# Kernel tuning notes

Hardware: AMD Instinct MI355X
Metric: run time of the kernel (lower is better)

## Reference

```python
import jax, jax.numpy as jnp
import numpy as np
from jax import lax

SIGMA = 1.5
KSIZE = 11  # int(6*1.5+1)=10 -> even -> 11
PAD = KSIZE // 2


def _gaussian_kernel_3d(ksize: int, sigma: float, dtype=jnp.float32):
    coords = jnp.arange(ksize, dtype=dtype) - (ksize // 2)
    g = jnp.exp(-(coords ** 2) / (2.0 * sigma ** 2))
    g = g / jnp.sum(g)
    # dense rank-1 separable outer product -> [k, k, k]
    k3 = g[:, None, None] * g[None, :, None] * g[None, None, :]
    return k3


def setup_inputs() -> dict:
    key = jax.random.key(0)
    x = jax.random.normal(key, (4, 1, 160, 192, 192), dtype=jnp.float32)
    return {"x": x}


def reference(x):
    # Faithful to torch: full dense 3D conv with the k^3 Gaussian kernel,
    # 'same' padding of kernel_size//2, single in/out channel.
    k3 = _gaussian_kernel_3d(KSIZE, SIGMA, x.dtype)
    w = k3[None, None]  # [O=1, I=1, kD, kH, kW]
    out = lax.conv_general_dilated(
        x, w,
        window_strides=(1, 1, 1),
        padding=[(PAD, PAD)] * 3,
        dimension_numbers=("NCDHW", "OIDHW", "NCDHW"),
    )
    return out
```

## Files before the change

kernel.cpp:

```cpp
#include <hip/hip_runtime.h>
#include <hip/hip_bf16.h>
#include <math.h>

#define KSIZE 11
#define PAD 5

struct GaussW { float w[KSIZE]; };

#define B_    4
#define D_    160
#define H_    192
#define W_    192
#define W4_   48

typedef float floatx4 __attribute__((ext_vector_type(4)));

#define TW4    16
#define TH     48
#define DCH    5
#define NH     (H_ / TH)
#define NWT    (W_ / (TW4*4))
#define NDC    (D_ / DCH)
#define NBLK_A (B_ * NH * NWT * NDC)
#define INROWS (TH + 10)
#define INW4   (TW4 + 4)
#define IN_STR4 21
#define WT_STR4 17
#define NSTAGE (INROWS * INW4)
#define PSTR4  (H_ * W4_)

static __device__ inline unsigned short f2bf(float f) {
    __hip_bfloat16 h = __float2bfloat16(f);
    return __builtin_bit_cast(unsigned short, h);
}
static __device__ inline float4 bf4_to_f4(ushort4 u) {
    return make_float4(__uint_as_float((unsigned)u.x << 16),
                       __uint_as_float((unsigned)u.y << 16),
                       __uint_as_float((unsigned)u.z << 16),
                       __uint_as_float((unsigned)u.w << 16));
}

__global__ __launch_bounds__(256) void blur_wh3(const float4* __restrict__ src,
                                                ushort4* __restrict__ wsb,
                                                GaussW g) {
    __shared__ __align__(16) float  lds_in[INROWS * IN_STR4 * 4];
    __shared__ __align__(16) ushort4 wtb[INROWS * WT_STR4];

    int bid = blockIdx.x;
    int L = (bid & 7) * (NBLK_A / 8) + (bid >> 3);
    int wx = L % NWT; L /= NWT;
    int hy = L % NH;  L /= NH;
    int dc = L % NDC;
    int b  = L / NDC;

    const int h0  = hy * TH;
    const int w0q = wx * TW4;
    const int d0  = dc * DCH;
    const int tid = threadIdx.x;

    const int wr   = tid >> 2;
    const int wq   = (tid & 3) * 4;
    const bool wact = (wr < INROWS);

    const int c4  = tid & 15;
    const int grp = tid >> 4;

    const float4* pin = src + (b * D_ + d0) * PSTR4;
    ushort4* pout = wsb + (b * D_ + d0) * PSTR4 + (h0 + 3 * grp) * W4_ + w0q + c4;

    float4 pf[5];
    auto issue = [&](const float4* plane) {
#pragma unroll
        for (int j = 0; j < 5; ++j) {
            pf[j] = make_float4(0.f, 0.f, 0.f, 0.f);
            int it = tid + j * 256;
            if (it < NSTAGE) {
                int ir = it / INW4, jc = it - ir * INW4;
                int h = h0 - PAD + ir;
                int q = w0q - 2 + jc;
                if (h >= 0 && h < H_ && q >= 0 && q < W4_)
                    pf[j] = plane[h * W4_ + q];
            }
        }
    };
    auto stage_write = [&]() {
#pragma unroll
        for (int j = 0; j < 5; ++j) {
            int it = tid + j * 256;
            if (it < NSTAGE) {
                int ir = it / INW4, jc = it - ir * INW4;
                *(float4*)&lds_in[(ir * IN_STR4 + jc) * 4] = pf[j];
            }
        }
    };

    issue(pin);
    stage_write();
    issue(pin + PSTR4);
    __syncthreads();

    for (int p = 0; p < DCH; ++p) {
        if (wact) {
            float win[32];
            const float* row = &lds_in[(wr * IN_STR4 + wq) * 4];
#pragma unroll
            for (int u = 0; u < 8; ++u) {
                float4 v = *(const float4*)&row[u * 4];
                win[4*u+0] = v.x; win[4*u+1] = v.y;
                win[4*u+2] = v.z; win[4*u+3] = v.w;
            }
            float o[16];
#pragma unroll
            for (int i = 0; i < 16; ++i) {
                float a = 0.f;
#pragma unroll
                for (int t = 0; t < KSIZE; ++t) a += g.w[t] * win[i + 3 + t];
                o[i] = a;
            }
            ushort4* wrow = &wtb[wr * WT_STR4 + wq];
#pragma unroll
            for (int c = 0; c < 4; ++c)
                wrow[c] = make_ushort4(f2bf(o[4*c]), f2bf(o[4*c+1]),
                                       f2bf(o[4*c+2]), f2bf(o[4*c+3]));
        }
        __syncthreads();

        if (p + 1 < DCH) stage_write();
        if (p + 2 < DCH) issue(pin + (p + 2) * PSTR4);

        {
            float4 a0 = make_float4(0.f,0.f,0.f,0.f);
            float4 a1 = a0, a2 = a0;
#pragma unroll
            for (int j = 0; j < 13; ++j) {
                float4 v = bf4_to_f4(wtb[(3*grp + j) * WT_STR4 + c4]);
                if (j <= 10) {
                    float wt_ = g.w[j];
                    a0.x += wt_*v.x; a0.y += wt_*v.y; a0.z += wt_*v.z; a0.w += wt_*v.w;
                }
                if (j >= 1 && j <= 11) {
                    float wt_ = g.w[j-1];
                    a1.x += wt_*v.x; a1.y += wt_*v.y; a1.z += wt_*v.z; a1.w += wt_*v.w;
                }
                if (j >= 2) {
                    float wt_ = g.w[j-2];
                    a2.x += wt_*v.x; a2.y += wt_*v.y; a2.z += wt_*v.z; a2.w += wt_*v.w;
                }
            }
            ushort4* op = pout + p * PSTR4;
            op[0      ] = make_ushort4(f2bf(a0.x), f2bf(a0.y), f2bf(a0.z), f2bf(a0.w));
            op[W4_    ] = make_ushort4(f2bf(a1.x), f2bf(a1.y), f2bf(a1.z), f2bf(a1.w));
            op[2 * W4_] = make_ushort4(f2bf(a2.x), f2bf(a2.y), f2bf(a2.z), f2bf(a2.w));
        }
        __syncthreads();
    }
}

template <int STR4, int LEN, int CH>
__global__ __launch_bounds__(256) void blur_d_slide(const ushort4* __restrict__ src,
                                                    float4* __restrict__ dst,
                                                    GaussW g, int ncol) {
    int tid = blockIdx.x * blockDim.x + threadIdx.x;
    int col = tid % ncol;
    int chunk = tid / ncol;
    int c0 = chunk * CH;
    int inner = col % STR4;
    int outer = col / STR4;
    int base = outer * (LEN * STR4) + inner;

    float4 ring[KSIZE];
#pragma unroll
    for (int j = 0; j < KSIZE - 1; ++j) {
        int cc = c0 - PAD + j;
        float4 v = make_float4(0.f, 0.f, 0.f, 0.f);
        if (cc >= 0 && cc < LEN) v = bf4_to_f4(src[base + cc * STR4]);
        ring[j] = v;
    }
#pragma unroll
    for (int k = 0; k < CH; ++k) {
        int cc = c0 + k + PAD;
        float4 v = make_float4(0.f, 0.f, 0.f, 0.f);
        if (cc < LEN) v = bf4_to_f4(src[base + cc * STR4]);
        ring[(KSIZE - 1 + k) % KSIZE] = v;

        float4 acc = make_float4(0.f, 0.f, 0.f, 0.f);
#pragma unroll
        for (int t = 0; t < KSIZE; ++t) {
            float4 u = ring[(k + t) % KSIZE];
            float wt = g.w[t];
            acc.x += wt * u.x; acc.y += wt * u.y;
            acc.z += wt * u.z; acc.w += wt * u.w;
        }
        floatx4 av; av.x = acc.x; av.y = acc.y; av.z = acc.z; av.w = acc.w;
        __builtin_nontemporal_store(av, (floatx4*)&dst[base + (c0 + k) * STR4]);
    }
}

__global__ void blur_dense_fallback(const float* __restrict__ src,
                                    float* __restrict__ dst,
                                    GaussW g, int B, int D, int H, int W) {
    long n = (long)B * D * H * W;
    long i = (long)blockIdx.x * blockDim.x + threadIdx.x;
    if (i >= n) return;
    int w = (int)(i % W);
    long r = i / W;
    int h = (int)(r % H); r /= H;
    int d = (int)(r % D);
    int b = (int)(r / D);

    float acc = 0.f;
    for (int td = 0; td < KSIZE; ++td) {
        int dd = d + td - PAD;
        if (dd < 0 || dd >= D) continue;
        for (int th = 0; th < KSIZE; ++th) {
            int hh = h + th - PAD;
            if (hh < 0 || hh >= H) continue;
            float wdh = g.w[td] * g.w[th];
            const float* row = src + (((long)b * D + dd) * H + hh) * W;
            for (int tw = 0; tw < KSIZE; ++tw) {
                int ww = w + tw - PAD;
                if (ww < 0 || ww >= W) continue;
                acc += wdh * g.w[tw] * row[ww];
            }
        }
    }
    dst[i] = acc;
}

extern "C" void kernel_launch(void* const* d_in, const int* in_sizes, int n_in,
                              void* d_out, int out_size, void* d_ws, size_t ws_size,
                              hipStream_t stream) {
    const float* x = (const float*)d_in[0];
    float* out = (float*)d_out;
    (void)in_sizes; (void)n_in; (void)out_size;

    const long n = (long)B_ * D_ * H_ * W_;

    GaussW g;
    {
        double tmp[KSIZE], s = 0.0;
        for (int i = 0; i < KSIZE; ++i) {
            double dd = (double)(i - PAD);
            tmp[i] = exp(-(dd * dd) / (2.0 * 1.5 * 1.5));
            s += tmp[i];
        }
        for (int i = 0; i < KSIZE; ++i) g.w[i] = (float)(tmp[i] / s);
    }

    if (ws_size >= (size_t)n * sizeof(unsigned short)) {
        blur_wh3<<<NBLK_A, 256, 0, stream>>>((const float4*)x, (ushort4*)d_ws, g);
        const int ncol = B_ * H_ * W4_;
        const int threads = ncol * (D_ / 16);
        blur_d_slide<9216, 160, 16><<<threads / 256, 256, 0, stream>>>(
            (const ushort4*)d_ws, (float4*)out, g, ncol);
    } else {
        long gridN = (n + 255) / 256;
        blur_dense_fallback<<<(int)gridN, 256, 0, stream>>>(x, out, g, B_, D_, H_, W_);
    }
}
```

Measured before the change: 57.47 us.

## Reorder passes: depth blur first to bf16, then fused W/H blur to fp32

Swaps the order of the separable passes. The depth pass now reads fp32 input and writes a bf16 intermediate, and the tiled W/H pass reads bf16 from LDS-staged planes and writes the fp32 output with nontemporal stores. The aim is to move the W/H kernel's halo-heavy staging traffic onto the half-width bf16 intermediate and give it smaller LDS tiles. Total DRAM bytes stay roughly the same, so any gain depends on halo re-reads and LDS footprint. Rounding now happens after the depth pass rather than after W/H, which slightly changes the numerics.

Result: slower. 58.91 us (+2.5%).

```diff
diff --git a/kernel.cpp b/kernel.cpp
--- a/kernel.cpp
+++ b/kernel.cpp
@@ -14,6 +14,57 @@
 #define W4_   48
 
 typedef float floatx4 __attribute__((ext_vector_type(4)));
+
+static __device__ inline unsigned short f2bf(float f) {
+    __hip_bfloat16 h = __float2bfloat16(f);
+    return __builtin_bit_cast(unsigned short, h);
+}
+static __device__ inline float4 bf4_to_f4(ushort4 u) {
+    return make_float4(__uint_as_float((unsigned)u.x << 16),
+                       __uint_as_float((unsigned)u.y << 16),
+                       __uint_as_float((unsigned)u.z << 16),
+                       __uint_as_float((unsigned)u.w << 16));
+}
+
+template <int STR4, int LEN, int CH>
+__global__ __launch_bounds__(256) void blur_d_f32bf(const float4* __restrict__ src,
+                                                    ushort4* __restrict__ dst,
+                                                    GaussW g, int ncol) {
+    int tid = blockIdx.x * blockDim.x + threadIdx.x;
+    int col = tid % ncol;
+    int chunk = tid / ncol;
+    int c0 = chunk * CH;
+    int inner = col % STR4;
+    int outer = col / STR4;
+    int base = outer * (LEN * STR4) + inner;
+
+    float4 ring[KSIZE];
+#pragma unroll
+    for (int j = 0; j < KSIZE - 1; ++j) {
+        int cc = c0 - PAD + j;
+        float4 v = make_float4(0.f, 0.f, 0.f, 0.f);
+        if (cc >= 0 && cc < LEN) v = src[base + cc * STR4];
+        ring[j] = v;
+    }
+#pragma unroll
+    for (int k = 0; k < CH; ++k) {
+        int cc = c0 + k + PAD;
+        float4 v = make_float4(0.f, 0.f, 0.f, 0.f);
+        if (cc < LEN) v = src[base + cc * STR4];
+        ring[(KSIZE - 1 + k) % KSIZE] = v;
+
+        float4 acc = make_float4(0.f, 0.f, 0.f, 0.f);
+#pragma unroll
+        for (int t = 0; t < KSIZE; ++t) {
+            float4 u = ring[(k + t) % KSIZE];
+            float wt = g.w[t];
+            acc.x += wt * u.x; acc.y += wt * u.y;
+            acc.z += wt * u.z; acc.w += wt * u.w;
+        }
+        dst[base + (c0 + k) * STR4] =
+            make_ushort4(f2bf(acc.x), f2bf(acc.y), f2bf(acc.z), f2bf(acc.w));
+    }
+}
 
 #define TW4    16
 #define TH     48
@@ -29,21 +80,10 @@
 #define NSTAGE (INROWS * INW4)
 #define PSTR4  (H_ * W4_)
 
-static __device__ inline unsigned short f2bf(float f) {
-    __hip_bfloat16 h = __float2bfloat16(f);
-    return __builtin_bit_cast(unsigned short, h);
-}
-static __device__ inline float4 bf4_to_f4(ushort4 u) {
-    return make_float4(__uint_as_float((unsigned)u.x << 16),
-                       __uint_as_float((unsigned)u.y << 16),
-                       __uint_as_float((unsigned)u.z << 16),
-                       __uint_as_float((unsigned)u.w << 16));
-}
-
-__global__ __launch_bounds__(256) void blur_wh3(const float4* __restrict__ src,
-                                                ushort4* __restrict__ wsb,
-                                                GaussW g) {
-    __shared__ __align__(16) float  lds_in[INROWS * IN_STR4 * 4];
+__global__ __launch_bounds__(256) void blur_wh_bf(const ushort4* __restrict__ src,
+                                                  float4* __restrict__ dst,
+                                                  GaussW g) {
+    __shared__ __align__(16) ushort4 lds_in[INROWS * IN_STR4];
     __shared__ __align__(16) ushort4 wtb[INROWS * WT_STR4];
 
     int bid = blockIdx.x;
@@ -65,14 +105,14 @@
     const int c4  = tid & 15;
     const int grp = tid >> 4;
 
-    const float4* pin = src + (b * D_ + d0) * PSTR4;
-    ushort4* pout = wsb + (b * D_ + d0) * PSTR4 + (h0 + 3 * grp) * W4_ + w0q + c4;
-
-    float4 pf[5];
-    auto issue = [&](const float4* plane) {
+    const ushort4* pin = src + (b * D_ + d0) * PSTR4;
+    float4* pout = dst + (b * D_ + d0) * PSTR4 + (h0 + 3 * grp) * W4_ + w0q + c4;
+
+    ushort4 pf[5];
+    auto issue = [&](const ushort4* plane) {
 #pragma unroll
         for (int j = 0; j < 5; ++j) {
-            pf[j] = make_float4(0.f, 0.f, 0.f, 0.f);
+            pf[j] = make_ushort4(0, 0, 0, 0);
             int it = tid + j * 256;
             if (it < NSTAGE) {
                 int ir = it / INW4, jc = it - ir * INW4;
@@ -89,7 +129,7 @@
             int it = tid + j * 256;
             if (it < NSTAGE) {
                 int ir = it / INW4, jc = it - ir * INW4;
-                *(float4*)&lds_in[(ir * IN_STR4 + jc) * 4] = pf[j];
+                lds_in[ir * IN_STR4 + jc] = pf[j];
             }
         }
     };
@@ -102,10 +142,10 @@
     for (int p = 0; p < DCH; ++p) {
         if (wact) {
             float win[32];
-            const float* row = &lds_in[(wr * IN_STR4 + wq) * 4];
+            const ushort4* row = &lds_in[wr * IN_STR4 + wq];
 #pragma unroll
             for (int u = 0; u < 8; ++u) {
-                float4 v = *(const float4*)&row[u * 4];
+                float4 v = bf4_to_f4(row[u]);
                 win[4*u+0] = v.x; win[4*u+1] = v.y;
                 win[4*u+2] = v.z; win[4*u+3] = v.w;
             }
@@ -147,52 +187,15 @@
                     a2.x += wt_*v.x; a2.y += wt_*v.y; a2.z += wt_*v.z; a2.w += wt_*v.w;
                 }
             }
-            ushort4* op = pout + p * PSTR4;
-            op[0      ] = make_ushort4(f2bf(a0.x), f2bf(a0.y), f2bf(a0.z), f2bf(a0.w));
-            op[W4_    ] = make_ushort4(f2bf(a1.x), f2bf(a1.y), f2bf(a1.z), f2bf(a1.w));
-            op[2 * W4_] = make_ushort4(f2bf(a2.x), f2bf(a2.y), f2bf(a2.z), f2bf(a2.w));
+            float4* op = pout + p * PSTR4;
+            floatx4 v0; v0.x = a0.x; v0.y = a0.y; v0.z = a0.z; v0.w = a0.w;
+            floatx4 v1; v1.x = a1.x; v1.y = a1.y; v1.z = a1.z; v1.w = a1.w;
+            floatx4 v2; v2.x = a2.x; v2.y = a2.y; v2.z = a2.z; v2.w = a2.w;
+            __builtin_nontemporal_store(v0, (floatx4*)&op[0]);
+            __builtin_nontemporal_store(v1, (floatx4*)&op[W4_]);
+            __builtin_nontemporal_store(v2, (floatx4*)&op[2 * W4_]);
         }
         __syncthreads();
-    }
-}
-
-template <int STR4, int LEN, int CH>
-__global__ __launch_bounds__(256) void blur_d_slide(const ushort4* __restrict__ src,
-                                                    float4* __restrict__ dst,
-                                                    GaussW g, int ncol) {
-    int tid = blockIdx.x * blockDim.x + threadIdx.x;
-    int col = tid % ncol;
-    int chunk = tid / ncol;
-    int c0 = chunk * CH;
-    int inner = col % STR4;
-    int outer = col / STR4;
-    int base = outer * (LEN * STR4) + inner;
-
-    float4 ring[KSIZE];
-#pragma unroll
-    for (int j = 0; j < KSIZE - 1; ++j) {
-        int cc = c0 - PAD + j;
-        float4 v = make_float4(0.f, 0.f, 0.f, 0.f);
-        if (cc >= 0 && cc < LEN) v = bf4_to_f4(src[base + cc * STR4]);
-        ring[j] = v;
-    }
-#pragma unroll
-    for (int k = 0; k < CH; ++k) {
-        int cc = c0 + k + PAD;
-        float4 v = make_float4(0.f, 0.f, 0.f, 0.f);
-        if (cc < LEN) v = bf4_to_f4(src[base + cc * STR4]);
-        ring[(KSIZE - 1 + k) % KSIZE] = v;
-
-        float4 acc = make_float4(0.f, 0.f, 0.f, 0.f);
-#pragma unroll
-        for (int t = 0; t < KSIZE; ++t) {
-            float4 u = ring[(k + t) % KSIZE];
-            float wt = g.w[t];
-            acc.x += wt * u.x; acc.y += wt * u.y;
-            acc.z += wt * u.z; acc.w += wt * u.w;
-        }
-        floatx4 av; av.x = acc.x; av.y = acc.y; av.z = acc.z; av.w = acc.w;
-        __builtin_nontemporal_store(av, (floatx4*)&dst[base + (c0 + k) * STR4]);
     }
 }
 
@@ -248,11 +251,13 @@
     }
 
     if (ws_size >= (size_t)n * sizeof(unsigned short)) {
-        blur_wh3<<<NBLK_A, 256, 0, stream>>>((const float4*)x, (ushort4*)d_ws, g);
-        const int ncol = B_ * H_ * W4_;
-        const int threads = ncol * (D_ / 16);
-        blur_d_slide<9216, 160, 16><<<threads / 256, 256, 0, stream>>>(
-            (const ushort4*)d_ws, (float4*)out, g, ncol);
+        {
+            const int ncol = B_ * H_ * W4_;
+            const int threads = ncol * (D_ / 16);
+            blur_d_f32bf<9216, 160, 16><<<threads / 256, 256, 0, stream>>>(
+                (const float4*)x, (ushort4*)d_ws, g, ncol);
+        }
+        blur_wh_bf<<<NBLK_A, 256, 0, stream>>>((const ushort4*)d_ws, (float4*)out, g);
     } else {
         long gridN = (n + 255) / 256;
         blur_dense_fallback<<<(int)gridN, 256, 0, stream>>>(x, out, g, B_, D_, H_, W_);
```
